# Kernel optimization log

Measured on AMD Instinct MI355X. Metric: run time of the kernel, lower is better.

## Reference

```python
import jax, jax.numpy as jnp
import numpy as np

B, T, D, H = 8192, 65, 32, 128  # batch, time points, state dim, hidden dim
DT = 0.1  # spacing of the shared time grid


def setup_inputs() -> dict:
    key = jax.random.key(0)
    k0, k1, k2 = jax.random.split(key, 3)
    x = jax.random.normal(k0, (B, T, D), dtype=jnp.float32)
    # shared, strictly increasing time grid (only t[0] is used by the model)
    t = jnp.broadcast_to(jnp.arange(T, dtype=jnp.float32) * DT, (B, T))
    itv = jnp.zeros((B, T), dtype=jnp.int32)       # unused in nn/intervention=False path
    itv_mask = jnp.zeros((B, T), dtype=jnp.int32)  # unused
    # nn.init.normal_(weight, std=0.1), bias = 0
    W1 = (jax.random.normal(k1, (H, D), dtype=jnp.float32) * 0.1)
    b1 = jnp.zeros((H,), dtype=jnp.float32)
    W2 = (jax.random.normal(k2, (D, H), dtype=jnp.float32) * 0.1)
    b2 = jnp.zeros((D,), dtype=jnp.float32)
    return dict(x=x, t=t, itv=itv, itv_mask=itv_mask, W1=W1, b1=b1, W2=W2, b2=b2)


def reference(x, t, itv, itv_mask, W1, b1, W2, b2):
    # drift: Linear -> Tanh -> Linear (autonomous; t is ignored by NN.forward)
    def f(y):
        return jnp.tanh(y @ W1.T + b1) @ W2.T + b2

    # one Dormand-Prince (dopri5) step of size h (5th-order solution, b7 = 0)
    def dopri5_step(y, h):
        k1 = f(y)
        k2 = f(y + h * (0.2 * k1))
        k3 = f(y + h * (3.0 / 40.0 * k1 + 9.0 / 40.0 * k2))
        k4 = f(y + h * (44.0 / 45.0 * k1 - 56.0 / 15.0 * k2 + 32.0 / 9.0 * k3))
        k5 = f(y + h * (19372.0 / 6561.0 * k1 - 25360.0 / 2187.0 * k2
                        + 64448.0 / 6561.0 * k3 - 212.0 / 729.0 * k4))
        k6 = f(y + h * (9017.0 / 3168.0 * k1 - 355.0 / 33.0 * k2
                        + 46732.0 / 5247.0 * k3 + 49.0 / 176.0 * k4
                        - 5103.0 / 18656.0 * k5))
        return y + h * (35.0 / 384.0 * k1 + 500.0 / 1113.0 * k3
                        + 125.0 / 192.0 * k4 - 2187.0 / 6784.0 * k5
                        + 11.0 / 84.0 * k6)

    y0 = x[:, 0, :]          # [B, D]
    ts = t[0]                # shared grid, [T]
    hs = ts[1:] - ts[:-1]    # [T-1] step sizes

    def scan_fn(y, h):
        y_next = dopri5_step(y, h)
        return y_next, y_next

    _, ys = jax.lax.scan(scan_fn, y0, hs)              # [T-1, B, D]
    pred = jnp.concatenate([y0[None], ys], axis=0)     # [T, B, D]
    return pred.transpose(1, 0, 2)                     # [B, T, D]
```

## Files before the change

kernel.cpp:

```cpp
#include <hip/hip_runtime.h>

#define TT 65
#define NSTEP 64

typedef __attribute__((ext_vector_type(8))) short bf16x8;
typedef __attribute__((ext_vector_type(4))) float f32x4;
typedef __attribute__((ext_vector_type(4))) unsigned int u32x4;

#define MFMA32(A,B,C) __builtin_amdgcn_mfma_f32_16x16x32_bf16((A),(B),(C),0,0,0)

#if __has_builtin(__builtin_amdgcn_exp2f)
#define EXP2F(x) __builtin_amdgcn_exp2f(x)
#else
#define EXP2F(x) __expf(0.6931471805599453f * (x))
#endif

__device__ constexpr float ATc[6][5] = {
    {0.f, 0.f, 0.f, 0.f, 0.f},
    {0.2f, 0.f, 0.f, 0.f, 0.f},
    {3.f/40.f, 9.f/40.f, 0.f, 0.f, 0.f},
    {44.f/45.f, -56.f/15.f, 32.f/9.f, 0.f, 0.f},
    {19372.f/6561.f, -25360.f/2187.f, 64448.f/6561.f, -212.f/729.f, 0.f},
    {9017.f/3168.f, -355.f/33.f, 46732.f/5247.f, 49.f/176.f, -5103.f/18656.f}
};
__device__ constexpr float BTc[6] = {35.f/384.f, 0.f, 500.f/1113.f, 125.f/192.f,
                                     -2187.f/6784.f, 11.f/84.f};

__device__ __forceinline__ float tanh_fast(float x) {
    float e = EXP2F(x * 2.8853900817779268f);
    return fmaf(-2.0f, __builtin_amdgcn_rcpf(e + 1.0f), 1.0f);
}

__device__ __forceinline__ void barrier_lds() {
    asm volatile("s_waitcnt lgkmcnt(0)" ::: "memory");
    __builtin_amdgcn_s_barrier();
}

__device__ __forceinline__ unsigned int permhi(unsigned int b, unsigned int a) {
    return __builtin_amdgcn_perm(b, a, 0x07060302u);
}
__device__ __forceinline__ unsigned int packpair_init(float a, float b) {
    return permhi(__float_as_uint(b) + 0x8000u, __float_as_uint(a) + 0x8000u);
}
__device__ __forceinline__ bf16x8 pack8(const float* v) {
    u32x4 H = {packpair_init(v[0], v[1]), packpair_init(v[2], v[3]),
               packpair_init(v[4], v[5]), packpair_init(v[6], v[7])};
    return __builtin_bit_cast(bf16x8, H);
}

__device__ __forceinline__ unsigned int cvtpk(float a, float b) {
    unsigned int r;
    asm("v_cvt_pk_bf16_f32 %0, %1, %2" : "=v"(r) : "v"(a), "v"(b));
    return r;
}
__device__ __forceinline__ bf16x8 packz(f32x4 a, f32x4 b) {
    u32x4 H = {cvtpk(a[0], a[1]), cvtpk(a[2], a[3]),
               cvtpk(b[0], b[1]), cvtpk(b[2], b[3])};
    return __builtin_bit_cast(bf16x8, H);
}

__global__ __launch_bounds__(256, 2)
void NeuralODE_dopri5_r16(const float* __restrict__ x, const float* __restrict__ tptr,
                          const float* __restrict__ W1, const float* __restrict__ b1,
                          const float* __restrict__ W2, const float* __restrict__ b2,
                          float* __restrict__ out)
{
    __shared__ unsigned int ytp[16][16];
    __shared__ __align__(16) float pb[4][512];

    const int tid = threadIdx.x;
    const int w   = tid >> 6;
    const int l   = tid & 63;
    const int r   = l & 15;
    const int q   = l >> 4;
    const int g   = (r >> 1) & 3;
    const int swz = (r & 7) << 2;
    const int row = blockIdx.x * 16 + r;
    const int d0  = 8 * w + 2 * q;

    bf16x8 W1f[2];
    f32x4 b1f[2];
    {
        float v[8];
        #pragma unroll
        for (int i = 0; i < 2; ++i) {
            int m = 2 * w + i;
            *(f32x4*)&v[0] = *(const f32x4*)&W1[(16*m + r) * 32 + 8*q];
            *(f32x4*)&v[4] = *(const f32x4*)&W1[(16*m + r) * 32 + 8*q + 4];
            W1f[i] = pack8(v);
            b1f[i] = *(const f32x4*)&b1[16*m + 4*q];
        }
    }
    bf16x8 W2f[2];
    {
        float v[8];
        #pragma unroll
        for (int dt = 0; dt < 2; ++dt) {
            *(f32x4*)&v[0] = *(const f32x4*)&W2[(16*dt + r) * 128 + 32*w + 4*q];
            *(f32x4*)&v[4] = *(const f32x4*)&W2[(16*dt + r) * 128 + 32*w + 16 + 4*q];
            W2f[dt] = pack8(v);
        }
    }
    const f32x4 zero = {0.f, 0.f, 0.f, 0.f};
    f32x4 acc_init[2];
    #pragma unroll
    for (int dt = 0; dt < 2; ++dt)
        acc_init[dt] = (w == 0) ? *(const f32x4*)&b2[16*dt + 4*q] : zero;

    unsigned int* const ytw = &ytp[r][((w ^ g) << 2) + q];
    const u32x4* const ytr  = (const u32x4*)&ytp[r][(q ^ g) << 2];
    float* const pbw0 = &pb[w][r * 32 + ((     4*q) ^ swz)];
    float* const pbw1 = &pb[w][r * 32 + ((16 + 4*q) ^ swz)];
    const float* const pred = &pb[0][r * 32 + (d0 ^ swz)];

    const float h_all = tptr[l + 1] - tptr[l];

    float2 y0 = *(const float2*)&x[(size_t)row * (TT*32) + d0];
    float yx = y0.x, yy = y0.y;
    *ytw = cvtpk(yx, yy);
    *(float2*)&out[(size_t)row * (TT*32) + d0] = y0;
    float kxs[5], kys[5];
    barrier_lds();

    #pragma unroll 1
    for (int step = 0; step < NSTEP; ++step) {
        const float h = __shfl(h_all, step);
        float bax = 0.f, bay = 0.f;

        #pragma unroll
        for (int s = 0; s < 6; ++s) {
            bf16x8 B1 = __builtin_bit_cast(bf16x8, *ytr);

            f32x4 z0 = MFMA32(W1f[0], B1, b1f[0]);
            f32x4 z1 = MFMA32(W1f[1], B1, b1f[1]);
            #pragma unroll
            for (int e = 0; e < 4; ++e) { z0[e] = tanh_fast(z0[e]); z1[e] = tanh_fast(z1[e]); }

            bf16x8 Zh = packz(z0, z1);

            f32x4 p0 = MFMA32(W2f[0], Zh, acc_init[0]);
            f32x4 p1 = MFMA32(W2f[1], Zh, acc_init[1]);
            *(f32x4*)pbw0 = p0;
            *(f32x4*)pbw1 = p1;
            barrier_lds();

            float2 pp0 = *(const float2*)&pred[0 * 512];
            float2 pp1 = *(const float2*)&pred[1 * 512];
            float2 pp2 = *(const float2*)&pred[2 * 512];
            float2 pp3 = *(const float2*)&pred[3 * 512];
            float kx = (pp0.x + pp1.x) + (pp2.x + pp3.x);
            float ky = (pp0.y + pp1.y) + (pp2.y + pp3.y);
            if (s < 5) { kxs[s] = kx; kys[s] = ky; }
            bax = fmaf(BTc[s], kx, bax);
            bay = fmaf(BTc[s], ky, bay);

            float ytx, yty;
            if (s < 5) {
                float ax = ATc[s+1][s] * kx;
                float ay = ATc[s+1][s] * ky;
                #pragma unroll
                for (int j = 0; j < 5; ++j)
                    if (j < s) { ax = fmaf(ATc[s+1][j], kxs[j], ax);
                                 ay = fmaf(ATc[s+1][j], kys[j], ay); }
                ytx = fmaf(h, ax, yx);
                yty = fmaf(h, ay, yy);
            } else {
                yx = fmaf(h, bax, yx);
                yy = fmaf(h, bay, yy);
                ytx = yx; yty = yy;
                float2 yn = {yx, yy};
                *(float2*)&out[(size_t)row * (TT*32) + (size_t)(step+1) * 32 + d0] = yn;
            }
            *ytw = cvtpk(ytx, yty);
            barrier_lds();
        }
    }
}

extern "C" void kernel_launch(void* const* d_in, const int* in_sizes, int n_in,
                              void* d_out, int out_size, void* d_ws, size_t ws_size,
                              hipStream_t stream) {
    (void)in_sizes; (void)n_in; (void)d_ws; (void)ws_size; (void)out_size;
    const float* x  = (const float*)d_in[0];
    const float* t  = (const float*)d_in[1];
    const float* W1 = (const float*)d_in[4];
    const float* b1 = (const float*)d_in[5];
    const float* W2 = (const float*)d_in[6];
    const float* b2 = (const float*)d_in[7];
    float* out = (float*)d_out;

    dim3 grid(8192 / 16);
    dim3 block(256);
    hipLaunchKernelGGL(NeuralODE_dopri5_r16, grid, block, 0, stream,
                       x, t, W1, b1, W2, b2, out);
}
```

Measured before the change: 220.1 us.

## Run each 16-row tile on a single wavefront with register-resident MLP and bpermute

Moves the whole hidden layer and the second-layer reduction of a 16-row batch tile into one 64-lane wavefront instead of four, so each thread holds all eight W1 fragments and all W2 fragments in registers. The cross-wave partial-sum reduction through LDS and the two block barriers per stage go away. The state transpose that feeds the next MFMA is now done with ds_bpermute. The cost is much higher register pressure and four times more MFMA and tanh work per wave, with only 512 single-wave blocks, which lowers occupancy and latency hiding.

After: 280.6 us. 1.27x slower.

```diff
diff --git a/kernel.cpp b/kernel.cpp
--- a/kernel.cpp
+++ b/kernel.cpp
@@ -31,11 +31,6 @@
     return fmaf(-2.0f, __builtin_amdgcn_rcpf(e + 1.0f), 1.0f);
 }
 
-__device__ __forceinline__ void barrier_lds() {
-    asm volatile("s_waitcnt lgkmcnt(0)" ::: "memory");
-    __builtin_amdgcn_s_barrier();
-}
-
 __device__ __forceinline__ unsigned int permhi(unsigned int b, unsigned int a) {
     return __builtin_amdgcn_perm(b, a, 0x07060302u);
 }
@@ -59,120 +54,152 @@
     return __builtin_bit_cast(bf16x8, H);
 }
 
-__global__ __launch_bounds__(256, 2)
-void NeuralODE_dopri5_r16(const float* __restrict__ x, const float* __restrict__ tptr,
+__device__ __forceinline__ f32x4 fma4s(float c, f32x4 a, f32x4 b) {
+    f32x4 r;
+    #pragma unroll
+    for (int i = 0; i < 4; ++i) r[i] = fmaf(c, a[i], b[i]);
+    return r;
+}
+
+__global__ __launch_bounds__(64, 1)
+void NeuralODE_dopri5_r17(const float* __restrict__ x, const float* __restrict__ tptr,
                           const float* __restrict__ W1, const float* __restrict__ b1,
                           const float* __restrict__ W2, const float* __restrict__ b2,
                           float* __restrict__ out)
 {
-    __shared__ unsigned int ytp[16][16];
-    __shared__ __align__(16) float pb[4][512];
-
-    const int tid = threadIdx.x;
-    const int w   = tid >> 6;
-    const int l   = tid & 63;
-    const int r   = l & 15;
-    const int q   = l >> 4;
-    const int g   = (r >> 1) & 3;
-    const int swz = (r & 7) << 2;
+    const int l = threadIdx.x;
+    const int r = l & 15;
+    const int q = l >> 4;
     const int row = blockIdx.x * 16 + r;
-    const int d0  = 8 * w + 2 * q;
-
-    bf16x8 W1f[2];
-    f32x4 b1f[2];
-    {
+
+    bf16x8 W1f[8];
+    f32x4 b1f[8];
+    #pragma unroll
+    for (int m = 0; m < 8; ++m) {
         float v[8];
+        *(f32x4*)&v[0] = *(const f32x4*)&W1[(16*m + r) * 32 + 8*q];
+        *(f32x4*)&v[4] = *(const f32x4*)&W1[(16*m + r) * 32 + 8*q + 4];
+        W1f[m] = pack8(v);
+        b1f[m] = *(const f32x4*)&b1[16*m + 4*q];
+    }
+    bf16x8 W2f[2][4];
+    f32x4 b2f[2];
+    #pragma unroll
+    for (int dt = 0; dt < 2; ++dt) {
+        b2f[dt] = *(const f32x4*)&b2[16*dt + 4*q];
         #pragma unroll
-        for (int i = 0; i < 2; ++i) {
-            int m = 2 * w + i;
-            *(f32x4*)&v[0] = *(const f32x4*)&W1[(16*m + r) * 32 + 8*q];
-            *(f32x4*)&v[4] = *(const f32x4*)&W1[(16*m + r) * 32 + 8*q + 4];
-            W1f[i] = pack8(v);
-            b1f[i] = *(const f32x4*)&b1[16*m + 4*q];
+        for (int kf = 0; kf < 4; ++kf) {
+            float v[8];
+            *(f32x4*)&v[0] = *(const f32x4*)&W2[(16*dt + r) * 128 + 32*kf + 4*q];
+            *(f32x4*)&v[4] = *(const f32x4*)&W2[(16*dt + r) * 128 + 32*kf + 16 + 4*q];
+            W2f[dt][kf] = pack8(v);
         }
     }
-    bf16x8 W2f[2];
-    {
-        float v[8];
-        #pragma unroll
-        for (int dt = 0; dt < 2; ++dt) {
-            *(f32x4*)&v[0] = *(const f32x4*)&W2[(16*dt + r) * 128 + 32*w + 4*q];
-            *(f32x4*)&v[4] = *(const f32x4*)&W2[(16*dt + r) * 128 + 32*w + 16 + 4*q];
-            W2f[dt] = pack8(v);
-        }
-    }
+
+    const int a01 = 4 * ((q & 1) * 32 + r);
+    const int a23 = a01 + 64;
+    const bool hiq = (q >= 2);
+
+    const float h_all = tptr[l + 1] - tptr[l];
+
+    f32x4 y0v = *(const f32x4*)&x[(size_t)row * (TT*32) + 4*q];
+    f32x4 y1v = *(const f32x4*)&x[(size_t)row * (TT*32) + 16 + 4*q];
+    *(f32x4*)&out[(size_t)row * (TT*32) + 4*q]      = y0v;
+    *(f32x4*)&out[(size_t)row * (TT*32) + 16 + 4*q] = y1v;
+
+    unsigned int P0  = cvtpk(y0v[0], y0v[1]);
+    unsigned int P1  = cvtpk(y0v[2], y0v[3]);
+    unsigned int P2c = cvtpk(y1v[0], y1v[1]);
+    unsigned int P3  = cvtpk(y1v[2], y1v[3]);
+
+    f32x4 kk0[5], kk1[5];
     const f32x4 zero = {0.f, 0.f, 0.f, 0.f};
-    f32x4 acc_init[2];
-    #pragma unroll
-    for (int dt = 0; dt < 2; ++dt)
-        acc_init[dt] = (w == 0) ? *(const f32x4*)&b2[16*dt + 4*q] : zero;
-
-    unsigned int* const ytw = &ytp[r][((w ^ g) << 2) + q];
-    const u32x4* const ytr  = (const u32x4*)&ytp[r][(q ^ g) << 2];
-    float* const pbw0 = &pb[w][r * 32 + ((     4*q) ^ swz)];
-    float* const pbw1 = &pb[w][r * 32 + ((16 + 4*q) ^ swz)];
-    const float* const pred = &pb[0][r * 32 + (d0 ^ swz)];
-
-    const float h_all = tptr[l + 1] - tptr[l];
-
-    float2 y0 = *(const float2*)&x[(size_t)row * (TT*32) + d0];
-    float yx = y0.x, yy = y0.y;
-    *ytw = cvtpk(yx, yy);
-    *(float2*)&out[(size_t)row * (TT*32) + d0] = y0;
-    float kxs[5], kys[5];
-    barrier_lds();
 
     #pragma unroll 1
     for (int step = 0; step < NSTEP; ++step) {
         const float h = __shfl(h_all, step);
-        float bax = 0.f, bay = 0.f;
+        f32x4 ba0 = zero, ba1 = zero;
 
         #pragma unroll
         for (int s = 0; s < 6; ++s) {
-            bf16x8 B1 = __builtin_bit_cast(bf16x8, *ytr);
+            int w0a = __builtin_amdgcn_ds_bpermute(a01, (int)P0);
+            int w0b = __builtin_amdgcn_ds_bpermute(a01, (int)P2c);
+            int w1a = __builtin_amdgcn_ds_bpermute(a01, (int)P1);
+            int w1b = __builtin_amdgcn_ds_bpermute(a01, (int)P3);
+            int w2a = __builtin_amdgcn_ds_bpermute(a23, (int)P0);
+            int w2b = __builtin_amdgcn_ds_bpermute(a23, (int)P2c);
+            int w3a = __builtin_amdgcn_ds_bpermute(a23, (int)P1);
+            int w3b = __builtin_amdgcn_ds_bpermute(a23, (int)P3);
+            u32x4 Bw = { (unsigned int)(hiq ? w0b : w0a),
+                         (unsigned int)(hiq ? w1b : w1a),
+                         (unsigned int)(hiq ? w2b : w2a),
+                         (unsigned int)(hiq ? w3b : w3a) };
+            bf16x8 B1 = __builtin_bit_cast(bf16x8, Bw);
 
             f32x4 z0 = MFMA32(W1f[0], B1, b1f[0]);
             f32x4 z1 = MFMA32(W1f[1], B1, b1f[1]);
+            f32x4 z2 = MFMA32(W1f[2], B1, b1f[2]);
+            f32x4 z3 = MFMA32(W1f[3], B1, b1f[3]);
+            f32x4 z4 = MFMA32(W1f[4], B1, b1f[4]);
+            f32x4 z5 = MFMA32(W1f[5], B1, b1f[5]);
+            f32x4 z6 = MFMA32(W1f[6], B1, b1f[6]);
+            f32x4 z7 = MFMA32(W1f[7], B1, b1f[7]);
             #pragma unroll
-            for (int e = 0; e < 4; ++e) { z0[e] = tanh_fast(z0[e]); z1[e] = tanh_fast(z1[e]); }
-
-            bf16x8 Zh = packz(z0, z1);
-
-            f32x4 p0 = MFMA32(W2f[0], Zh, acc_init[0]);
-            f32x4 p1 = MFMA32(W2f[1], Zh, acc_init[1]);
-            *(f32x4*)pbw0 = p0;
-            *(f32x4*)pbw1 = p1;
-            barrier_lds();
-
-            float2 pp0 = *(const float2*)&pred[0 * 512];
-            float2 pp1 = *(const float2*)&pred[1 * 512];
-            float2 pp2 = *(const float2*)&pred[2 * 512];
-            float2 pp3 = *(const float2*)&pred[3 * 512];
-            float kx = (pp0.x + pp1.x) + (pp2.x + pp3.x);
-            float ky = (pp0.y + pp1.y) + (pp2.y + pp3.y);
-            if (s < 5) { kxs[s] = kx; kys[s] = ky; }
-            bax = fmaf(BTc[s], kx, bax);
-            bay = fmaf(BTc[s], ky, bay);
-
-            float ytx, yty;
+            for (int e = 0; e < 4; ++e) {
+                z0[e] = tanh_fast(z0[e]); z1[e] = tanh_fast(z1[e]);
+                z2[e] = tanh_fast(z2[e]); z3[e] = tanh_fast(z3[e]);
+                z4[e] = tanh_fast(z4[e]); z5[e] = tanh_fast(z5[e]);
+                z6[e] = tanh_fast(z6[e]); z7[e] = tanh_fast(z7[e]);
+            }
+
+            bf16x8 Zf0 = packz(z0, z1);
+            bf16x8 Zf1 = packz(z2, z3);
+            bf16x8 Zf2 = packz(z4, z5);
+            bf16x8 Zf3 = packz(z6, z7);
+
+            f32x4 k0, k1;
+            {
+                f32x4 pa = MFMA32(W2f[0][0], Zf0, b2f[0]);
+                pa       = MFMA32(W2f[0][1], Zf1, pa);
+                f32x4 pb = MFMA32(W2f[0][2], Zf2, zero);
+                pb       = MFMA32(W2f[0][3], Zf3, pb);
+                #pragma unroll
+                for (int e = 0; e < 4; ++e) k0[e] = pa[e] + pb[e];
+            }
+            {
+                f32x4 pa = MFMA32(W2f[1][0], Zf0, b2f[1]);
+                pa       = MFMA32(W2f[1][1], Zf1, pa);
+                f32x4 pb = MFMA32(W2f[1][2], Zf2, zero);
+                pb       = MFMA32(W2f[1][3], Zf3, pb);
+                #pragma unroll
+                for (int e = 0; e < 4; ++e) k1[e] = pa[e] + pb[e];
+            }
+
+            ba0 = fma4s(BTc[s], k0, ba0);
+            ba1 = fma4s(BTc[s], k1, ba1);
+
+            f32x4 yt0, yt1;
             if (s < 5) {
-                float ax = ATc[s+1][s] * kx;
-                float ay = ATc[s+1][s] * ky;
+                kk0[s] = k0; kk1[s] = k1;
+                f32x4 ax = zero, ay = zero;
                 #pragma unroll
                 for (int j = 0; j < 5; ++j)
-                    if (j < s) { ax = fmaf(ATc[s+1][j], kxs[j], ax);
-                                 ay = fmaf(ATc[s+1][j], kys[j], ay); }
-                ytx = fmaf(h, ax, yx);
-                yty = fmaf(h, ay, yy);
+                    if (j <= s) { ax = fma4s(ATc[s+1][j], kk0[j], ax);
+                                  ay = fma4s(ATc[s+1][j], kk1[j], ay); }
+                yt0 = fma4s(h, ax, y0v);
+                yt1 = fma4s(h, ay, y1v);
             } else {
-                yx = fmaf(h, bax, yx);
-                yy = fmaf(h, bay, yy);
-                ytx = yx; yty = yy;
-                float2 yn = {yx, yy};
-                *(float2*)&out[(size_t)row * (TT*32) + (size_t)(step+1) * 32 + d0] = yn;
-            }
-            *ytw = cvtpk(ytx, yty);
-            barrier_lds();
+                y0v = fma4s(h, ba0, y0v);
+                y1v = fma4s(h, ba1, y1v);
+                yt0 = y0v; yt1 = y1v;
+                size_t o = (size_t)row * (TT*32) + (size_t)(step + 1) * 32;
+                *(f32x4*)&out[o + 4*q]      = y0v;
+                *(f32x4*)&out[o + 16 + 4*q] = y1v;
+            }
+            P0  = cvtpk(yt0[0], yt0[1]);
+            P1  = cvtpk(yt0[2], yt0[3]);
+            P2c = cvtpk(yt1[0], yt1[1]);
+            P3  = cvtpk(yt1[2], yt1[3]);
         }
     }
 }
@@ -190,7 +217,7 @@
     float* out = (float*)d_out;
 
     dim3 grid(8192 / 16);
-    dim3 block(256);
-    hipLaunchKernelGGL(NeuralODE_dopri5_r16, grid, block, 0, stream,
+    dim3 block(64);
+    hipLaunchKernelGGL(NeuralODE_dopri5_r17, grid, block, 0, stream,
                        x, t, W1, b1, W2, b2, out);
 }
```
